# Kernel optimization log

Measured on AMD Instinct MI355X. Metric: run time of the kernel, lower is better.

The kernel has to match this reference:

```python
import jax, jax.numpy as jnp
import numpy as np

EMBED_DIM = 768
NUM_HEADS = 12
LORA_DIM = 64
HEAD_DIM = EMBED_DIM // NUM_HEADS
SCALING = float(HEAD_DIM) ** -0.5


def quick_gelu(x):
    return x * jax.nn.sigmoid(1.702 * x)


def setup_inputs() -> dict:
    key = jax.random.key(0)
    ks = jax.random.split(key, 12)
    bsz, tgt_len, E = 128, 197, EMBED_DIM
    x = jax.random.normal(ks[0], (bsz, tgt_len, E), dtype=jnp.float32)
    attn_mask = jnp.zeros((bsz, tgt_len, tgt_len), dtype=jnp.float32)
    top_idx = jax.random.randint(ks[1], (bsz,), 0, tgt_len)
    s = 0.02
    return {
        "x": x,
        "attn_mask": attn_mask,
        "in_proj_weight": jax.random.normal(ks[2], (3 * E, E)) * s,
        "in_proj_bias": jnp.zeros((3 * E,), jnp.float32),
        "out_proj_weight": jax.random.normal(ks[3], (E, E)) * s,
        "out_proj_bias": jnp.zeros((E,), jnp.float32),
        "lora_a": jax.random.normal(ks[4], (LORA_DIM, E)) * s,
        "lora_b": jax.random.normal(ks[5], (3 * E, LORA_DIM)) * s,
        "down_weight": jax.random.normal(ks[6], (LORA_DIM, E)) * s,
        "down_bias": jax.random.normal(ks[7], (LORA_DIM,)) * 1e-6,
        "up_weight": jax.random.normal(ks[8], (E, LORA_DIM)) * s,
        "up_bias": jnp.zeros((E,), jnp.float32),
        "n_f": 16,
        "top_idx": top_idx,
    }


def reference(x, attn_mask, in_proj_weight, in_proj_bias, out_proj_weight,
              out_proj_bias, lora_a, lora_b, down_weight, down_bias,
              up_weight, up_bias, n_f, top_idx):
    bsz, tgt_len, E = x.shape
    H, hd = NUM_HEADS, HEAD_DIM
    b = bsz // n_f

    # fused QKV + LoRA delta
    qkv = x @ in_proj_weight.T + in_proj_bias          # [bsz, L, 3E]
    qkv = qkv + (x @ lora_a.T) @ lora_b.T              # LoRA delta
    qkv = qkv.reshape(bsz, tgt_len, 3, H, hd)
    qkv = jnp.transpose(qkv, (2, 0, 3, 1, 4))          # [3, bsz, H, L, hd]
    q, k, v = qkv[0], qkv[1], qkv[2]

    # gather per-sample CLS query before scaling (matches torch order)
    q_1 = q[jnp.arange(bsz), :, top_idx, :]            # [bsz, H, hd]
    q_1 = jnp.transpose(q_1.reshape(b, n_f, H, hd), (0, 2, 1, 3))  # [b, H, f, hd]

    # frame-local attention
    attn = jnp.einsum('bhqd,bhkd->bhqk', q * SCALING, k) + attn_mask[:, None, :, :]
    attn = jax.nn.softmax(attn, axis=-1)
    xo = jnp.einsum('bhqk,bhkd->bhqd', attn, v)
    xo = jnp.transpose(xo, (0, 2, 1, 3)).reshape(bsz, tgt_len, E)
    xo = xo @ out_proj_weight.T + out_proj_bias        # [bsz, L, E]

    # global CLS attention over all frames' keys/values
    k_g = jnp.transpose(k.reshape(b, n_f, H, tgt_len, hd), (0, 2, 1, 3, 4)).reshape(b, H, n_f * tgt_len, hd)
    v_g = jnp.transpose(v.reshape(b, n_f, H, tgt_len, hd), (0, 2, 1, 3, 4)).reshape(b, H, n_f * tgt_len, hd)
    mask_g = attn_mask[:, -1, :].reshape(b, n_f * tgt_len)  # [b, f*L]

    attn_1 = jnp.einsum('bhfd,bhkd->bhfk', q_1 * SCALING, k_g) + mask_g[:, None, None, :]
    attn_1 = jax.nn.softmax(attn_1, axis=-1)
    x_1 = jnp.einsum('bhfk,bhkd->bhfd', attn_1, v_g)
    x_1 = jnp.transpose(x_1, (0, 2, 1, 3)).reshape(b, n_f, E)
    x_1 = x_1 @ out_proj_weight.T + out_proj_bias      # [b, f, E]

    # adapter on gathered CLS outputs
    x_0 = xo[jnp.arange(bsz), top_idx, :].reshape(b, n_f, E)
    x_0 = quick_gelu(x_0 @ down_weight.T + down_bias)
    x_0 = x_0 @ up_weight.T + up_bias                  # [b, f, E]

    update_cls = (x_0 + x_1).reshape(bsz, E)
    xo = xo.at[jnp.arange(bsz), top_idx, :].set(update_cls)
    return xo
```

## Files before the change

### kernel.cpp

```cpp
#include <hip/hip_runtime.h>
#include <hip/hip_bf16.h>

typedef __attribute__((ext_vector_type(4))) float f32x4;
typedef __attribute__((ext_vector_type(8))) short s16x8;

#define BSZ 128
#define TGT 197
#define EDIM 768
#define NH 12
#define HD 64
#define NF 16
#define M_TOT (BSZ*TGT)
#define QKV_N (3*EDIM)
#define KG (NF*TGT)
#define VSTR 264
#define NSPL 8
#define KSPL 394
#define LSTR 424

__device__ __forceinline__ float b2f(unsigned short u) {
  return __uint_as_float(((unsigned int)u) << 16);
}
__device__ __forceinline__ float bf2f(__hip_bfloat16 b) { return __bfloat162float(b); }
__device__ __forceinline__ __hip_bfloat16 f2bf(float f) { return __float2bfloat16(f); }
__device__ __forceinline__ unsigned int packbf(float a, float b) {
  __hip_bfloat16 x = __float2bfloat16(a), y = __float2bfloat16(b);
  return (unsigned int)*(unsigned short*)&x | ((unsigned int)*(unsigned short*)&y << 16);
}
__device__ __forceinline__ int swz(int t, int c) {
  return t*64 + (c ^ ((((t & 7) ^ ((t >> 3) & 3))) << 3));
}
__device__ __forceinline__ int vswz(int d, int t) {
  return d*VSTR + (t ^ (d & 56));
}

__device__ __forceinline__ void gload_lds16(const void* gsrc, void* ldst) {
  __builtin_amdgcn_global_load_lds(
      (const __attribute__((address_space(1))) unsigned int*)gsrc,
      (__attribute__((address_space(3))) unsigned int*)ldst, 16, 0, 0);
}

__global__ void detect_dtype(const unsigned short* __restrict__ xraw,
                             int* __restrict__ flag, int* __restrict__ mz) {
  if (threadIdx.x == 0 && blockIdx.x == 0) {
    float mx = 0.f;
    for (int j = 0; j < 1024; ++j) {
      float v = fabsf(b2f(xraw[j]));
      if (v < 1e30f) mx = fmaxf(mx, v);
      else mx = 1e30f;
    }
    *flag = (mx < 100.0f) ? 1 : 0;
    *mz = 1;
  }
}

__global__ __launch_bounds__(256) void detect_mask_zero(
    const unsigned int* __restrict__ mraw, int nelem,
    const int* __restrict__ flag, int* __restrict__ mz)
{
  const int isbf = *flag;
  const int nwords = isbf ? (nelem >> 1) : nelem;
  const unsigned int am = isbf ? 0x7fff7fffu : 0x7fffffffu;
  unsigned int acc = 0;
  for (int i = blockIdx.x*256 + threadIdx.x; i < nwords; i += gridDim.x*256)
    acc |= (mraw[i] & am);
  if (acc) atomicAnd(mz, 0);
}

__global__ __launch_bounds__(256) void convert_bf16(
    const void* __restrict__ src, __hip_bfloat16* __restrict__ dst,
    int n8, const int* __restrict__ flag, int skip_if_bf)
{
  const int isbf = *flag;
  if (skip_if_bf && isbf) return;
  int i = blockIdx.x * 256 + threadIdx.x;
  const int stride = gridDim.x * 256;
  if (isbf) {
    const s16x8* s = (const s16x8*)src;
    s16x8* d = (s16x8*)dst;
    for (; i < n8; i += stride) d[i] = s[i];
  } else {
    const f32x4* s = (const f32x4*)src;
    s16x8* d = (s16x8*)dst;
    for (; i < n8; i += stride) {
      f32x4 a = s[i*2], b = s[i*2+1];
      s16x8 o;
      #pragma unroll
      for (int j = 0; j < 4; ++j) { __hip_bfloat16 t = f2bf(a[j]); o[j] = *(short*)&t; }
      #pragma unroll
      for (int j = 0; j < 4; ++j) { __hip_bfloat16 t = f2bf(b[j]); o[4+j] = *(short*)&t; }
      d[i] = o;
    }
  }
}

struct CvBatch {
  const void* src[10];
  void* dst[10];
  int off8[11];
};

__global__ __launch_bounds__(256) void convert_batch(CvBatch cb, const int* __restrict__ flag)
{
  const int isbf = *flag;
  const int total = cb.off8[10];
  for (int i = blockIdx.x*256 + threadIdx.x; i < total; i += gridDim.x*256) {
    int s = 0;
    #pragma unroll
    for (int k = 1; k < 10; ++k) s += (i >= cb.off8[k]);
    const int li = i - cb.off8[s];
    if (isbf) {
      ((s16x8*)cb.dst[s])[li] = ((const s16x8*)cb.src[s])[li];
    } else {
      const f32x4* sp = (const f32x4*)cb.src[s];
      f32x4 a = sp[li*2], b = sp[li*2+1];
      s16x8 o;
      #pragma unroll
      for (int j = 0; j < 4; ++j) { __hip_bfloat16 t = f2bf(a[j]); o[j] = *(short*)&t; }
      #pragma unroll
      for (int j = 0; j < 4; ++j) { __hip_bfloat16 t = f2bf(b[j]); o[4+j] = *(short*)&t; }
      ((s16x8*)cb.dst[s])[li] = o;
    }
  }
}

__global__ __launch_bounds__(256) void build_wc(
    const __hip_bfloat16* __restrict__ W,
    const __hip_bfloat16* __restrict__ la,
    const __hip_bfloat16* __restrict__ lb,
    __hip_bfloat16* __restrict__ Wc)
{
  __shared__ float lbr[64];
  const int n = blockIdx.x;
  if (threadIdx.x < 64) lbr[threadIdx.x] = bf2f(lb[n*64 + threadIdx.x]);
  __syncthreads();
  for (int e = threadIdx.x; e < EDIM; e += 256) {
    float acc = bf2f(W[(size_t)n*EDIM + e]);
    for (int r = 0; r < 64; ++r) acc += lbr[r] * bf2f(la[r*EDIM + e]);
    Wc[(size_t)n*EDIM + e] = f2bf(acc);
  }
}

__global__ __launch_bounds__(512) void gemm_bt_8ph(
    const __hip_bfloat16* __restrict__ A,
    const __hip_bfloat16* __restrict__ A_alt,
    const __hip_bfloat16* __restrict__ B,
    const __hip_bfloat16* __restrict__ bias,
    void* __restrict__ C,
    int M, int N, int K, int ntiles,
    const int* __restrict__ flag, int flag_mode)
{
  __shared__ char lds[131072];
  const int tid = threadIdx.x;
  const int wave = tid >> 6, lane = tid & 63;
  const int l16 = lane & 15, kq = lane >> 4;
  const int wr = wave >> 2, wc2 = wave & 3;

  const int nwg = gridDim.x;
  const int bid = blockIdx.x;
  const int qc = nwg >> 3, rc = nwg & 7;
  const int xcd = bid & 7;
  const int wgid = (xcd < rc ? xcd*(qc+1) : rc*(qc+1) + (xcd-rc)*qc) + (bid >> 3);
  const long brow = (long)(wgid / ntiles) * 256;
  const long bcol = (long)(wgid % ntiles) * 256;

  const int isbf = *flag;
  const __hip_bfloat16* Ause = isbf ? A_alt : A;
  const int nkt = K >> 6;

  const int srow = tid >> 3;
  const int schunk = tid & 7;
  const int wuni = wave << 10;

  auto stA = [&](int t, int buf, int issue) {
    int ar = issue*64 + srow;
    int cs = schunk ^ (ar & 7);
    long gr = brow + ar; if (gr > (long)M - 1) gr = M - 1;
    gload_lds16(Ause + gr*(long)K + t*64 + cs*8,
                lds + buf*65536 + issue*8192 + wuni);
  };
  auto stB = [&](int t, int buf, int issue) {
    int br = issue*64 + srow;
    int cs = schunk ^ (br & 7);
    gload_lds16(B + (bcol + br)*(long)K + t*64 + cs*8,
                lds + buf*65536 + 32768 + issue*8192 + wuni);
  };
  auto rdA = [&](int buf, int q, int a, int ks) -> s16x8 {
    int ar = wr*128 + q*32 + a*16 + l16;
    int ch = ks*4 + kq;
    return *(const s16x8*)(lds + buf*65536 + ar*128 + ((ch ^ (ar & 7)) << 4));
  };
  auto rdB = [&](int buf, int ni, int ks) -> s16x8 {
    int br = wc2*64 + ni*16 + l16;
    int ch = ks*4 + kq;
    return *(const s16x8*)(lds + buf*65536 + 32768 + br*128 + ((ch ^ (br & 7)) << 4));
  };

  f32x4 acc[8][4];
  #pragma unroll
  for (int i = 0; i < 8; ++i)
    #pragma unroll
    for (int j = 0; j < 4; ++j) acc[i][j] = (f32x4){0.f,0.f,0.f,0.f};

  stB(0,0,0); stB(0,0,1); stB(0,0,2); stB(0,0,3);
  stA(0,0,0); stA(0,0,2); stA(0,0,1); stA(0,0,3);
  asm volatile("s_waitcnt vmcnt(2)" ::: "memory");
  __builtin_amdgcn_s_barrier();

  for (int t = 0; t < nkt; ++t) {
    const int cur = t & 1, nxt = cur ^ 1;
    const bool pf = (t + 1 < nkt);
    s16x8 bfr[4][2], af[2][2];

    #pragma unroll
    for (int ni = 0; ni < 4; ++ni) { bfr[ni][0] = rdB(cur,ni,0); bfr[ni][1] = rdB(cur,ni,1); }
    af[0][0]=rdA(cur,0,0,0); af[0][1]=rdA(cur,0,0,1);
    af[1][0]=rdA(cur,0,1,0); af[1][1]=rdA(cur,0,1,1);
    if (pf) { stB(t+1,nxt,0); stB(t+1,nxt,1); }
    __builtin_amdgcn_s_barrier();
    asm volatile("s_waitcnt lgkmcnt(0)" ::: "memory");
    __builtin_amdgcn_sched_barrier(0);
    __builtin_amdgcn_s_setprio(1);
    #pragma unroll
    for (int ks = 0; ks < 2; ++ks)
      #pragma unroll
      for (int ni = 0; ni < 4; ++ni) {
        acc[0][ni] = __builtin_amdgcn_mfma_f32_16x16x32_bf16(af[0][ks], bfr[ni][ks], acc[0][ni], 0,0,0);
        acc[1][ni] = __builtin_amdgcn_mfma_f32_16x16x32_bf16(af[1][ks], bfr[ni][ks], acc[1][ni], 0,0,0);
      }
    __builtin_amdgcn_s_setprio(0);

    af[0][0]=rdA(cur,1,0,0); af[0][1]=rdA(cur,1,0,1);
    af[1][0]=rdA(cur,1,1,0); af[1][1]=rdA(cur,1,1,1);
    if (pf) {
      stB(t+1,nxt,2); stB(t+1,nxt,3);
      asm volatile("s_waitcnt vmcnt(4)" ::: "memory");
    } else {
      asm volatile("s_waitcnt vmcnt(0)" ::: "memory");
    }
    __builtin_amdgcn_s_barrier();
    asm volatile("s_waitcnt lgkmcnt(0)" ::: "memory");
    __builtin_amdgcn_sched_barrier(0);
    __builtin_amdgcn_s_setprio(1);
    #pragma unroll
    for (int ks = 0; ks < 2; ++ks)
      #pragma unroll
      for (int ni = 0; ni < 4; ++ni) {
        acc[2][ni] = __builtin_amdgcn_mfma_f32_16x16x32_bf16(af[0][ks], bfr[ni][ks], acc[2][ni], 0,0,0);
        acc[3][ni] = __builtin_amdgcn_mfma_f32_16x16x32_bf16(af[1][ks], bfr[ni][ks], acc[3][ni], 0,0,0);
      }
    __builtin_amdgcn_s_setprio(0);

    af[0][0]=rdA(cur,2,0,0); af[0][1]=rdA(cur,2,0,1);
    af[1][0]=rdA(cur,2,1,0); af[1][1]=rdA(cur,2,1,1);
    if (pf) { stA(t+1,nxt,0); stA(t+1,nxt,2); }
    __builtin_amdgcn_s_barrier();
    asm volatile("s_waitcnt lgkmcnt(0)" ::: "memory");
    __builtin_amdgcn_sched_barrier(0);
    __builtin_amdgcn_s_setprio(1);
    #pragma unroll
    for (int ks = 0; ks < 2; ++ks)
      #pragma unroll
      for (int ni = 0; ni < 4; ++ni) {
        acc[4][ni] = __builtin_amdgcn_mfma_f32_16x16x32_bf16(af[0][ks], bfr[ni][ks], acc[4][ni], 0,0,0);
        acc[5][ni] = __builtin_amdgcn_mfma_f32_16x16x32_bf16(af[1][ks], bfr[ni][ks], acc[5][ni], 0,0,0);
      }
    __builtin_amdgcn_s_setprio(0);

    af[0][0]=rdA(cur,3,0,0); af[0][1]=rdA(cur,3,0,1);
    af[1][0]=rdA(cur,3,1,0); af[1][1]=rdA(cur,3,1,1);
    if (pf) { stA(t+1,nxt,1); stA(t+1,nxt,3); }
    asm volatile("s_waitcnt vmcnt(2)" ::: "memory");
    __builtin_amdgcn_s_barrier();
    asm volatile("s_waitcnt lgkmcnt(0)" ::: "memory");
    __builtin_amdgcn_sched_barrier(0);
    __builtin_amdgcn_s_setprio(1);
    #pragma unroll
    for (int ks = 0; ks < 2; ++ks)
      #pragma unroll
      for (int ni = 0; ni < 4; ++ni) {
        acc[6][ni] = __builtin_amdgcn_mfma_f32_16x16x32_bf16(af[0][ks], bfr[ni][ks], acc[6][ni], 0,0,0);
        acc[7][ni] = __builtin_amdgcn_mfma_f32_16x16x32_bf16(af[1][ks], bfr[ni][ks], acc[7][ni], 0,0,0);
      }
    __builtin_amdgcn_s_setprio(0);
  }

  __builtin_amdgcn_s_barrier();

  const int f32o = flag_mode && (!isbf);
  float bv[4];
  #pragma unroll
  for (int ni = 0; ni < 4; ++ni) bv[ni] = bf2f(bias[bcol + wc2*64 + ni*16 + l16]);
  const int o4 = kq*4;

  if (!f32o) {
    __hip_bfloat16* eb = (__hip_bfloat16*)(lds + wave*2048);
    __hip_bfloat16* Cb = (__hip_bfloat16*)C;
    const int rr = lane >> 3, cg = lane & 7;
    #pragma unroll
    for (int mi = 0; mi < 8; ++mi) {
      #pragma unroll
      for (int ni = 0; ni < 4; ++ni)
        #pragma unroll
        for (int r = 0; r < 4; ++r) {
          const int row16 = o4 + r;
          const int sidx = row16*64 + ((((ni*2 + (l16 >> 3)) ^ (row16 & 7)) << 3) | (l16 & 7));
          eb[sidx] = f2bf(acc[mi][ni][r] + bv[ni]);
        }
      asm volatile("s_waitcnt lgkmcnt(0)" ::: "memory");
      __builtin_amdgcn_sched_barrier(0);
      #pragma unroll
      for (int pass = 0; pass < 2; ++pass) {
        const int row16 = pass*8 + rr;
        const long grow = brow + wr*128 + mi*16 + row16;
        if (grow < M) {
          s16x8 v = *(const s16x8*)(eb + row16*64 + ((cg ^ (row16 & 7)) << 3));
          *(s16x8*)(Cb + grow*(long)N + bcol + wc2*64 + cg*8) = v;
        }
      }
      asm volatile("s_waitcnt lgkmcnt(0)" ::: "memory");
      __builtin_amdgcn_sched_barrier(0);
    }
  } else {
    #pragma unroll
    for (int mi = 0; mi < 8; ++mi)
      #pragma unroll
      for (int ni = 0; ni < 4; ++ni)
        #pragma unroll
        for (int r = 0; r < 4; ++r) {
          const long grow = brow + wr*128 + mi*16 + o4 + r;
          if (grow < M)
            ((float*)C)[grow*(long)N + bcol + wc2*64 + ni*16 + l16] = acc[mi][ni][r] + bv[ni];
        }
  }
}

__global__ __launch_bounds__(256) void attn_fused(
    const __hip_bfloat16* __restrict__ qkv,
    const __hip_bfloat16* __restrict__ mask,
    const __hip_bfloat16* __restrict__ mask_raw,
    const int* __restrict__ flag,
    const int* __restrict__ mzp,
    __hip_bfloat16* __restrict__ xop)
{
  __shared__ __hip_bfloat16 lVt[64*VSTR];

  const int tid = threadIdx.x;
  const int blk = blockIdx.x;
  const int xcd = blk & 7;
  const int slot = blk >> 3;
  const int ih = xcd * 192 + (slot >> 2);
  const int qt = slot & 3;
  const int h = ih % NH;
  const int i = ih / NH;
  const int q0 = qt * 64;
  const size_t rowbase = (size_t)i * TGT;
  const int wave = tid >> 6, lane = tid & 63;
  const int l16 = lane & 15, kq = lane >> 4;
  const int mz = *mzp;
  const __hip_bfloat16* msk = (*flag) ? mask_raw : mask;

  int qr = q0 + wave*16 + l16;
  const int qrc = qr > TGT-1 ? TGT-1 : qr;
  s16x8 qf[2];
  #pragma unroll
  for (int kk = 0; kk < 2; ++kk)
    qf[kk] = *(const s16x8*)(qkv + (rowbase + qrc)*QKV_N + h*HD + kk*32 + kq*8);

  const f32x4 z = {0.f,0.f,0.f,0.f};
  for (int idx = tid; idx < 224*8; idx += 256) {
    int t = idx >> 3, c8 = idx & 7;
    f32x4 vv = z;
    if (t < TGT) vv = *(const f32x4*)(qkv + (rowbase + t)*QKV_N + 2*EDIM + h*HD + c8*8);
    const __hip_bfloat16* pv = (const __hip_bfloat16*)&vv;
    const int tx = t ^ (c8 << 3);
    #pragma unroll
    for (int j = 0; j < 8; ++j)
      lVt[(c8*8 + j)*VSTR + tx] = pv[j];
  }
  __syncthreads();

  f32x4 acc[14];
  #pragma unroll
  for (int nf = 0; nf < 14; ++nf) {
    int trow = nf*16 + l16; if (trow > TGT-1) trow = TGT-1;
    acc[nf] = (f32x4){0.f,0.f,0.f,0.f};
    #pragma unroll
    for (int kk = 0; kk < 2; ++kk) {
      s16x8 kf = *(const s16x8*)(qkv + (rowbase + trow)*QKV_N + EDIM + h*HD + kk*32 + kq*8);
      acc[nf] = __builtin_amdgcn_mfma_f32_16x16x32_bf16(kf, qf[kk], acc[nf], 0, 0, 0);
    }
  }

  float mx = -1e30f;
  #pragma unroll
  for (int nf = 0; nf < 14; ++nf) {
    #pragma unroll
    for (int r = 0; r < 4; ++r) {
      const int t = nf*16 + kq*4 + r;
      float s;
      if (t < TGT) {
        s = acc[nf][r]*0.125f;
        if (!mz) s += bf2f(msk[(rowbase + qrc)*TGT + t]);
      } else s = -1e30f;
      acc[nf][r] = s;
      mx = fmaxf(mx, s);
    }
  }
  mx = fmaxf(mx, __shfl_xor(mx, 16));
  mx = fmaxf(mx, __shfl_xor(mx, 32));

  float rs = 0.f;
  unsigned int pk[14][2];
  #pragma unroll
  for (int nf = 0; nf < 14; ++nf) {
    float p0 = __expf(acc[nf][0] - mx);
    float p1 = __expf(acc[nf][1] - mx);
    float p2 = __expf(acc[nf][2] - mx);
    float p3 = __expf(acc[nf][3] - mx);
    rs += (p0 + p1) + (p2 + p3);
    pk[nf][0] = packbf(p0, p1);
    pk[nf][1] = packbf(p2, p3);
  }
  rs += __shfl_xor(rs, 16);
  rs += __shfl_xor(rs, 32);

  f32x4 oacc[4];
  #pragma unroll
  for (int nf = 0; nf < 4; ++nf) oacc[nf] = (f32x4){0.f,0.f,0.f,0.f};

  const int slbase = l16 + ((kq & 1) << 5);
  #pragma unroll
  for (int kt = 0; kt < 7; ++kt) {
    s16x8 pa;
    #pragma unroll
    for (int jp = 0; jp < 4; ++jp) {
      const int srcLane = slbase + ((jp >> 1) << 4);
      int va = __shfl((int)pk[2*kt][jp & 1], srcLane, 64);
      int vb = __shfl((int)pk[2*kt + 1][jp & 1], srcLane, 64);
      int sel = (kq < 2) ? va : vb;
      pa[2*jp]     = (short)(sel & 0xffff);
      pa[2*jp + 1] = (short)(((unsigned int)sel) >> 16);
    }
    #pragma unroll
    for (int nf = 0; nf < 4; ++nf) {
      s16x8 vf = *(const s16x8*)(lVt + vswz(nf*16 + l16, kt*32 + kq*8));
      oacc[nf] = __builtin_amdgcn_mfma_f32_16x16x32_bf16(pa, vf, oacc[nf], 0, 0, 0);
    }
  }

  #pragma unroll
  for (int r = 0; r < 4; ++r) {
    const float rsrc = __shfl(rs, kq*4 + r, 64);
    const int qw = q0 + wave*16 + kq*4 + r;
    if (qw < TGT) {
      const float inv = 1.0f / rsrc;
      #pragma unroll
      for (int nf = 0; nf < 4; ++nf)
        xop[(rowbase + qw)*(size_t)EDIM + h*HD + nf*16 + l16] = f2bf(oacc[nf][r] * inv);
    }
  }
}

__global__ __launch_bounds__(256) void cls_split(
    const __hip_bfloat16* __restrict__ qkv,
    const __hip_bfloat16* __restrict__ mask,
    const __hip_bfloat16* __restrict__ mask_raw,
    const int* __restrict__ flag,
    const int* __restrict__ mzp,
    const int* __restrict__ top_idx,
    float* __restrict__ pO,
    float* __restrict__ pm,
    float* __restrict__ pl)
{
  __shared__ __hip_bfloat16 lQ[16*64];
  __shared__ __hip_bfloat16 lS[16*LSTR];
  __shared__ __hip_bfloat16 lV[256*64];
  __shared__ float red[16][17];
  __shared__ float rmax[16];
  __shared__ float rsum[16];

  const int tid = threadIdx.x;
  const int sp = blockIdx.x & 7;
  const int gh = blockIdx.x >> 3;
  const int g = gh / NH;
  const int h = gh % NH;
  const int k0 = sp * KSPL;
  const int wave = tid >> 6, lane = tid & 63;
  const int l16 = lane & 15, kq = lane >> 4, o4 = (lane >> 4) * 4;
  const int mz = *mzp;
  const __hip_bfloat16* msk = (*flag) ? mask_raw : mask;

  if (tid < 128) {
    int qi = tid >> 3, c8 = tid & 7;
    int ib = g*NF + qi;
    int top = top_idx[ib];
    f32x4 v = *(const f32x4*)(qkv + ((size_t)ib*TGT + top)*QKV_N + h*HD + c8*8);
    *(f32x4*)(lQ + qi*64 + c8*8) = v;
  }
  __syncthreads();

  s16x8 q8[2];
  #pragma unroll
  for (int kk = 0; kk < 2; ++kk)
    q8[kk] = *(const s16x8*)(lQ + l16*64 + kk*32 + kq*8);

  for (int nf = wave; nf < 26; nf += 4) {
    const int keyl = nf*16 + l16;
    const int keyg = k0 + (keyl < KSPL ? keyl : 0);
    f32x4 a = {0.f,0.f,0.f,0.f};
    const size_t krow = (size_t)g*KG + keyg;
    #pragma unroll
    for (int kk = 0; kk < 2; ++kk) {
      s16x8 k8 = *(const s16x8*)(qkv + krow*QKV_N + EDIM + h*HD + kk*32 + kq*8);
      a = __builtin_amdgcn_mfma_f32_16x16x32_bf16(q8[kk], k8, a, 0, 0, 0);
    }
    float mval = 0.f;
    if (!mz && keyl < KSPL) {
      const int f = keyg / 197;
      const int t = keyg - f*197;
      mval = bf2f(msk[((size_t)(g*NF + f)*TGT + (TGT-1))*TGT + t]);
    }
    #pragma unroll
    for (int r = 0; r < 4; ++r)
      lS[(o4 + r)*LSTR + nf*16 + l16] = f2bf(keyl < KSPL ? a[r]*0.125f + mval : -1e30f);
  }
  __syncthreads();

  {
    const int q = tid >> 4, c = tid & 15;
    float mx = -1e30f;
    for (int gch = c; gch < 52; gch += 16) {
      s16x8 sv = *(const s16x8*)(lS + q*LSTR + gch*8);
      #pragma unroll
      for (int j = 0; j < 8; ++j) mx = fmaxf(mx, b2f((unsigned short)sv[j]));
    }
    red[q][c] = mx;
    __syncthreads();
    if (tid < 16) {
      float m = red[tid][0];
      for (int j = 1; j < 16; ++j) m = fmaxf(m, red[tid][j]);
      rmax[tid] = m;
    }
    __syncthreads();
    const float rowmax = rmax[q];
    float sum = 0.f;
    for (int gch = c; gch < 52; gch += 16) {
      s16x8 sv = *(const s16x8*)(lS + q*LSTR + gch*8);
      s16x8 ov;
      #pragma unroll
      for (int jp = 0; jp < 4; ++jp) {
        float e0 = __expf(b2f((unsigned short)sv[2*jp])   - rowmax);
        float e1 = __expf(b2f((unsigned short)sv[2*jp+1]) - rowmax);
        sum += e0 + e1;
        unsigned int pr = packbf(e0, e1);
        ov[2*jp]   = (short)(pr & 0xffff);
        ov[2*jp+1] = (short)(pr >> 16);
      }
      *(s16x8*)(lS + q*LSTR + gch*8) = ov;
    }
    red[q][c] = sum;
    __syncthreads();
    if (tid < 16) {
      float s = 0.f;
      for (int j = 0; j < 16; ++j) s += red[tid][j];
      rsum[tid] = s;
    }
  }

  f32x4 oa = {0.f,0.f,0.f,0.f};
  const f32x4 z = {0.f,0.f,0.f,0.f};
  #pragma unroll
  for (int cki = 0; cki < 2; ++cki) {
    const int ck = cki * 256;
    const int nrows = cki ? 160 : 256;
    const int nks = cki ? 5 : 8;
    __syncthreads();
    for (int idx = tid; idx < nrows*8; idx += 256) {
      int t2 = idx >> 3, c8 = idx & 7;
      int keyl = ck + t2;
      f32x4 v = z;
      if (keyl < KSPL)
        v = *(const f32x4*)(qkv + ((size_t)g*KG + k0 + keyl)*QKV_N + 2*EDIM + h*HD + c8*8);
      *(f32x4*)(lV + swz(t2, c8*8)) = v;
    }
    __syncthreads();
    for (int ks = 0; ks < nks; ++ks) {
      s16x8 pa = *(const s16x8*)(lS + l16*LSTR + ck + ks*32 + kq*8);
      s16x8 vf;
      #pragma unroll
      for (int j = 0; j < 8; ++j) {
        const int t2 = ks*32 + kq*8 + j;
        vf[j] = *(const short*)(lV + swz(t2, wave*16 + l16));
      }
      oa = __builtin_amdgcn_mfma_f32_16x16x32_bf16(pa, vf, oa, 0, 0, 0);
    }
  }

  const int ps = gh*NSPL + sp;
  #pragma unroll
  for (int r = 0; r < 4; ++r)
    pO[((size_t)ps*16 + (o4 + r))*64 + wave*16 + l16] = oa[r];
  if (tid < 16) {
    pm[ps*16 + tid] = rmax[tid];
    pl[ps*16 + tid] = rsum[tid];
  }
}

__global__ __launch_bounds__(256) void cls_combine(
    const float* __restrict__ pO,
    const float* __restrict__ pm,
    const float* __restrict__ pl,
    __hip_bfloat16* __restrict__ x1buf)
{
  __shared__ float M[16];
  __shared__ float L[16];
  __shared__ float sc[NSPL][16];
  const int tid = threadIdx.x;
  const int gh = blockIdx.x;
  const int g = gh / NH;
  const int h = gh % NH;

  if (tid < 16) {
    float m = -1e30f;
    for (int s = 0; s < NSPL; ++s) m = fmaxf(m, pm[(gh*NSPL + s)*16 + tid]);
    M[tid] = m;
  }
  __syncthreads();
  if (tid < 128) {
    const int s = tid >> 4, q = tid & 15;
    sc[s][q] = __expf(pm[(gh*NSPL + s)*16 + q] - M[q]);
  }
  __syncthreads();
  if (tid < 16) {
    float l = 0.f;
    for (int s = 0; s < NSPL; ++s) l += pl[(gh*NSPL + s)*16 + tid] * sc[s][tid];
    L[tid] = l;
  }
  __syncthreads();
  for (int idx = tid; idx < 16*64; idx += 256) {
    const int q = idx >> 6, d = idx & 63;
    float acc = 0.f;
    for (int s = 0; s < NSPL; ++s)
      acc += pO[((size_t)(gh*NSPL + s)*16 + q)*64 + d] * sc[s][q];
    x1buf[((size_t)(g*NF + q))*EDIM + h*64 + d] = f2bf(acc / L[q]);
  }
}

__global__ __launch_bounds__(256) void final_update(
    void* __restrict__ out,
    const __hip_bfloat16* __restrict__ x1p,
    const __hip_bfloat16* __restrict__ dw, const __hip_bfloat16* __restrict__ db,
    const __hip_bfloat16* __restrict__ uw, const __hip_bfloat16* __restrict__ ub,
    const int* __restrict__ top_idx, const int* __restrict__ flag)
{
  __shared__ float x0[EDIM];
  __shared__ float hmid[64];
  const int i = blockIdx.x;
  const int tid = threadIdx.x;
  const int top = top_idx[i];
  const int isbf = *flag;
  const size_t rowoff = ((size_t)i*TGT + top)*EDIM;
  for (int e = tid; e < EDIM; e += 256)
    x0[e] = isbf ? bf2f(((const __hip_bfloat16*)out)[rowoff + e])
                 : ((const float*)out)[rowoff + e];
  __syncthreads();
  if (tid < 64) {
    float a = bf2f(db[tid]);
    for (int e = 0; e < EDIM; ++e) a += x0[e] * bf2f(dw[tid*EDIM + e]);
    hmid[tid] = a / (1.f + __expf(-1.702f * a));
  }
  __syncthreads();
  for (int e = tid; e < EDIM; e += 256) {
    float a = bf2f(ub[e]) + bf2f(x1p[(size_t)i*EDIM + e]);
    #pragma unroll
    for (int r = 0; r < 64; ++r) a += hmid[r] * bf2f(uw[e*64 + r]);
    if (isbf) ((__hip_bfloat16*)out)[rowoff + e] = f2bf(a);
    else ((float*)out)[rowoff + e] = a;
  }
}

extern "C" void kernel_launch(void* const* d_in, const int* in_sizes, int n_in,
                              void* d_out, int out_size, void* d_ws, size_t ws_size,
                              hipStream_t stream) {
  (void)in_sizes; (void)n_in; (void)out_size; (void)ws_size;
  const int* top_idx = (const int*)d_in[13];
  const __hip_bfloat16* x_raw    = (const __hip_bfloat16*)d_in[0];
  const __hip_bfloat16* mask_raw = (const __hip_bfloat16*)d_in[1];

  char* ws = (char*)d_ws;
  size_t off = 0;
  auto alloc = [&](size_t bytes) { char* p = ws + off; off += (bytes + 15) & ~(size_t)15; return p; };

  int* flag = (int*)alloc(16);
  int* mz   = (int*)alloc(16);
  __hip_bfloat16* x_c    = (__hip_bfloat16*)alloc((size_t)19365888*2);
  __hip_bfloat16* mask_c = (__hip_bfloat16*)alloc((size_t)4967552*2);
  __hip_bfloat16* wIn_c  = (__hip_bfloat16*)alloc((size_t)1769472*2);
  __hip_bfloat16* bIn_c  = (__hip_bfloat16*)alloc((size_t)2304*2);
  __hip_bfloat16* wOut_c = (__hip_bfloat16*)alloc((size_t)589824*2);
  __hip_bfloat16* bOut_c = (__hip_bfloat16*)alloc((size_t)768*2);
  __hip_bfloat16* la_c   = (__hip_bfloat16*)alloc((size_t)49152*2);
  __hip_bfloat16* lb_c   = (__hip_bfloat16*)alloc((size_t)147456*2);
  __hip_bfloat16* dw_c   = (__hip_bfloat16*)alloc((size_t)49152*2);
  __hip_bfloat16* db_c   = (__hip_bfloat16*)alloc((size_t)64*2);
  __hip_bfloat16* uw_c   = (__hip_bfloat16*)alloc((size_t)49152*2);
  __hip_bfloat16* ub_c   = (__hip_bfloat16*)alloc((size_t)768*2);
  __hip_bfloat16* Wc     = (__hip_bfloat16*)alloc((size_t)QKV_N*EDIM*2);
  __hip_bfloat16* qkv    = (__hip_bfloat16*)alloc((size_t)M_TOT*QKV_N*2);
  __hip_bfloat16* xop    = (__hip_bfloat16*)alloc((size_t)M_TOT*EDIM*2);
  __hip_bfloat16* x1b    = (__hip_bfloat16*)alloc((size_t)BSZ*EDIM*2);
  __hip_bfloat16* x1p    = (__hip_bfloat16*)alloc((size_t)BSZ*EDIM*2);
  float* pO = (float*)alloc((size_t)96*NSPL*16*64*4);
  float* pm = (float*)alloc((size_t)96*NSPL*16*4);
  float* pl = (float*)alloc((size_t)96*NSPL*16*4);

  detect_dtype<<<1, 64, 0, stream>>>((const unsigned short*)d_in[0], flag, mz);
  detect_mask_zero<<<2048, 256, 0, stream>>>((const unsigned int*)d_in[1], 4967552, flag, mz);

  convert_bf16<<<2048, 256, 0, stream>>>(d_in[0], x_c, 19365888/8, flag, 1);
  convert_bf16<<<2048, 256, 0, stream>>>(d_in[1], mask_c, 4967552/8, flag, 1);

  CvBatch cb;
  const int srcIdx[10] = {2,3,4,5,6,7,8,9,10,11};
  void* dsts[10] = {wIn_c, bIn_c, wOut_c, bOut_c, la_c, lb_c, dw_c, db_c, uw_c, ub_c};
  const int ns[10] = {1769472, 2304, 589824, 768, 49152, 147456, 49152, 64, 49152, 768};
  int cum = 0;
  for (int k = 0; k < 10; ++k) {
    cb.src[k] = d_in[srcIdx[k]];
    cb.dst[k] = dsts[k];
    cb.off8[k] = cum;
    cum += ns[k] / 8;
  }
  cb.off8[10] = cum;
  convert_batch<<<(cum + 255)/256, 256, 0, stream>>>(cb, flag);

  build_wc<<<2304, 256, 0, stream>>>(wIn_c, la_c, lb_c, Wc);

  gemm_bt_8ph<<<99*9, 512, 0, stream>>>(x_c, x_raw, Wc, bIn_c, qkv,
                                        M_TOT, QKV_N, EDIM, 9, flag, 0);
  attn_fused<<<dim3(6144), 256, 0, stream>>>(qkv, mask_c, mask_raw, flag, mz, xop);
  cls_split<<<dim3(96*NSPL), 256, 0, stream>>>(qkv, mask_c, mask_raw, flag, mz,
                                               top_idx, pO, pm, pl);
  gemm_bt_8ph<<<99*3, 512, 0, stream>>>(xop, xop, wOut_c, bOut_c, d_out,
                                        M_TOT, EDIM, EDIM, 3, flag, 1);
  cls_combine<<<dim3(96), 256, 0, stream>>>(pO, pm, pl, x1b);
  gemm_bt_8ph<<<3, 512, 0, stream>>>(x1b, x1b, wOut_c, bOut_c, x1p,
                                     BSZ, EDIM, EDIM, 3, flag, 0);
  final_update<<<128, 256, 0, stream>>>(d_out, x1p, dw_c, db_c, uw_c, ub_c, top_idx, flag);
}
```

Measured before the change: 469.9 us.

## Merge out-projection GEMM and CLS split attention into one heterogeneous launch

Combines the out-projection GEMM and the split-K CLS global attention into one kernel. The first 297 blocks run the GEMM and the rest run the CLS split work, so the small CLS workload fills CUs left idle by the GEMM tail and one launch is removed. In exchange, the CLS blocks now use 512-thread blocks with half the threads idle and inherit the GEMM's 128KB shared-memory allocation, which may lower occupancy for that part.

After: 462.7 us. About the same (-1.5%).

```diff
diff --git a/kernel.cpp b/kernel.cpp
--- a/kernel.cpp
+++ b/kernel.cpp
@@ -17,6 +17,7 @@
 #define NSPL 8
 #define KSPL 394
 #define LSTR 424
+#define NGEMM_OP 297
 
 __device__ __forceinline__ float b2f(unsigned short u) {
   return __uint_as_float(((unsigned int)u) << 16);
@@ -335,6 +336,348 @@
   }
 }
 
+__global__ __launch_bounds__(512) void outproj_cls(
+    const __hip_bfloat16* __restrict__ A,
+    const __hip_bfloat16* __restrict__ B,
+    const __hip_bfloat16* __restrict__ bias,
+    void* __restrict__ C,
+    const __hip_bfloat16* __restrict__ qkv,
+    const __hip_bfloat16* __restrict__ mask,
+    const __hip_bfloat16* __restrict__ mask_raw,
+    const int* __restrict__ flag,
+    const int* __restrict__ mzp,
+    const int* __restrict__ top_idx,
+    float* __restrict__ pO,
+    float* __restrict__ pm,
+    float* __restrict__ pl)
+{
+  __shared__ char lds[131072];
+  const int tid = threadIdx.x;
+  const int wave = tid >> 6, lane = tid & 63;
+  const int l16 = lane & 15, kq = lane >> 4;
+  const int isbf = *flag;
+
+  if (blockIdx.x < NGEMM_OP) {
+    const int wr = wave >> 2, wc2 = wave & 3;
+    const int M = M_TOT, N = EDIM, K = EDIM, ntiles = 3;
+    const int nwg = NGEMM_OP;
+    const int bid = blockIdx.x;
+    const int qc = nwg >> 3, rc = nwg & 7;
+    const int xcd = bid & 7;
+    const int wgid = (xcd < rc ? xcd*(qc+1) : rc*(qc+1) + (xcd-rc)*qc) + (bid >> 3);
+    const long brow = (long)(wgid / ntiles) * 256;
+    const long bcol = (long)(wgid % ntiles) * 256;
+    const int nkt = K >> 6;
+
+    const int srow = tid >> 3;
+    const int schunk = tid & 7;
+    const int wuni = wave << 10;
+
+    auto stA = [&](int t, int buf, int issue) {
+      int ar = issue*64 + srow;
+      int cs = schunk ^ (ar & 7);
+      long gr = brow + ar; if (gr > (long)M - 1) gr = M - 1;
+      gload_lds16(A + gr*(long)K + t*64 + cs*8,
+                  lds + buf*65536 + issue*8192 + wuni);
+    };
+    auto stB = [&](int t, int buf, int issue) {
+      int br = issue*64 + srow;
+      int cs = schunk ^ (br & 7);
+      gload_lds16(B + (bcol + br)*(long)K + t*64 + cs*8,
+                  lds + buf*65536 + 32768 + issue*8192 + wuni);
+    };
+    auto rdA = [&](int buf, int q, int a, int ks) -> s16x8 {
+      int ar = wr*128 + q*32 + a*16 + l16;
+      int ch = ks*4 + kq;
+      return *(const s16x8*)(lds + buf*65536 + ar*128 + ((ch ^ (ar & 7)) << 4));
+    };
+    auto rdB = [&](int buf, int ni, int ks) -> s16x8 {
+      int br = wc2*64 + ni*16 + l16;
+      int ch = ks*4 + kq;
+      return *(const s16x8*)(lds + buf*65536 + 32768 + br*128 + ((ch ^ (br & 7)) << 4));
+    };
+
+    f32x4 acc[8][4];
+    #pragma unroll
+    for (int i = 0; i < 8; ++i)
+      #pragma unroll
+      for (int j = 0; j < 4; ++j) acc[i][j] = (f32x4){0.f,0.f,0.f,0.f};
+
+    stB(0,0,0); stB(0,0,1); stB(0,0,2); stB(0,0,3);
+    stA(0,0,0); stA(0,0,2); stA(0,0,1); stA(0,0,3);
+    asm volatile("s_waitcnt vmcnt(2)" ::: "memory");
+    __builtin_amdgcn_s_barrier();
+
+    for (int t = 0; t < nkt; ++t) {
+      const int cur = t & 1, nxt = cur ^ 1;
+      const bool pf = (t + 1 < nkt);
+      s16x8 bfr[4][2], af[2][2];
+
+      #pragma unroll
+      for (int ni = 0; ni < 4; ++ni) { bfr[ni][0] = rdB(cur,ni,0); bfr[ni][1] = rdB(cur,ni,1); }
+      af[0][0]=rdA(cur,0,0,0); af[0][1]=rdA(cur,0,0,1);
+      af[1][0]=rdA(cur,0,1,0); af[1][1]=rdA(cur,0,1,1);
+      if (pf) { stB(t+1,nxt,0); stB(t+1,nxt,1); }
+      __builtin_amdgcn_s_barrier();
+      asm volatile("s_waitcnt lgkmcnt(0)" ::: "memory");
+      __builtin_amdgcn_sched_barrier(0);
+      __builtin_amdgcn_s_setprio(1);
+      #pragma unroll
+      for (int ks = 0; ks < 2; ++ks)
+        #pragma unroll
+        for (int ni = 0; ni < 4; ++ni) {
+          acc[0][ni] = __builtin_amdgcn_mfma_f32_16x16x32_bf16(af[0][ks], bfr[ni][ks], acc[0][ni], 0,0,0);
+          acc[1][ni] = __builtin_amdgcn_mfma_f32_16x16x32_bf16(af[1][ks], bfr[ni][ks], acc[1][ni], 0,0,0);
+        }
+      __builtin_amdgcn_s_setprio(0);
+
+      af[0][0]=rdA(cur,1,0,0); af[0][1]=rdA(cur,1,0,1);
+      af[1][0]=rdA(cur,1,1,0); af[1][1]=rdA(cur,1,1,1);
+      if (pf) {
+        stB(t+1,nxt,2); stB(t+1,nxt,3);
+        asm volatile("s_waitcnt vmcnt(4)" ::: "memory");
+      } else {
+        asm volatile("s_waitcnt vmcnt(0)" ::: "memory");
+      }
+      __builtin_amdgcn_s_barrier();
+      asm volatile("s_waitcnt lgkmcnt(0)" ::: "memory");
+      __builtin_amdgcn_sched_barrier(0);
+      __builtin_amdgcn_s_setprio(1);
+      #pragma unroll
+      for (int ks = 0; ks < 2; ++ks)
+        #pragma unroll
+        for (int ni = 0; ni < 4; ++ni) {
+          acc[2][ni] = __builtin_amdgcn_mfma_f32_16x16x32_bf16(af[0][ks], bfr[ni][ks], acc[2][ni], 0,0,0);
+          acc[3][ni] = __builtin_amdgcn_mfma_f32_16x16x32_bf16(af[1][ks], bfr[ni][ks], acc[3][ni], 0,0,0);
+        }
+      __builtin_amdgcn_s_setprio(0);
+
+      af[0][0]=rdA(cur,2,0,0); af[0][1]=rdA(cur,2,0,1);
+      af[1][0]=rdA(cur,2,1,0); af[1][1]=rdA(cur,2,1,1);
+      if (pf) { stA(t+1,nxt,0); stA(t+1,nxt,2); }
+      __builtin_amdgcn_s_barrier();
+      asm volatile("s_waitcnt lgkmcnt(0)" ::: "memory");
+      __builtin_amdgcn_sched_barrier(0);
+      __builtin_amdgcn_s_setprio(1);
+      #pragma unroll
+      for (int ks = 0; ks < 2; ++ks)
+        #pragma unroll
+        for (int ni = 0; ni < 4; ++ni) {
+          acc[4][ni] = __builtin_amdgcn_mfma_f32_16x16x32_bf16(af[0][ks], bfr[ni][ks], acc[4][ni], 0,0,0);
+          acc[5][ni] = __builtin_amdgcn_mfma_f32_16x16x32_bf16(af[1][ks], bfr[ni][ks], acc[5][ni], 0,0,0);
+        }
+      __builtin_amdgcn_s_setprio(0);
+
+      af[0][0]=rdA(cur,3,0,0); af[0][1]=rdA(cur,3,0,1);
+      af[1][0]=rdA(cur,3,1,0); af[1][1]=rdA(cur,3,1,1);
+      if (pf) { stA(t+1,nxt,1); stA(t+1,nxt,3); }
+      asm volatile("s_waitcnt vmcnt(2)" ::: "memory");
+      __builtin_amdgcn_s_barrier();
+      asm volatile("s_waitcnt lgkmcnt(0)" ::: "memory");
+      __builtin_amdgcn_sched_barrier(0);
+      __builtin_amdgcn_s_setprio(1);
+      #pragma unroll
+      for (int ks = 0; ks < 2; ++ks)
+        #pragma unroll
+        for (int ni = 0; ni < 4; ++ni) {
+          acc[6][ni] = __builtin_amdgcn_mfma_f32_16x16x32_bf16(af[0][ks], bfr[ni][ks], acc[6][ni], 0,0,0);
+          acc[7][ni] = __builtin_amdgcn_mfma_f32_16x16x32_bf16(af[1][ks], bfr[ni][ks], acc[7][ni], 0,0,0);
+        }
+      __builtin_amdgcn_s_setprio(0);
+    }
+
+    __builtin_amdgcn_s_barrier();
+
+    float bv[4];
+    #pragma unroll
+    for (int ni = 0; ni < 4; ++ni) bv[ni] = bf2f(bias[bcol + wc2*64 + ni*16 + l16]);
+    const int o4 = kq*4;
+
+    if (isbf) {
+      __hip_bfloat16* eb = (__hip_bfloat16*)(lds + wave*2048);
+      __hip_bfloat16* Cb = (__hip_bfloat16*)C;
+      const int rr = lane >> 3, cg = lane & 7;
+      #pragma unroll
+      for (int mi = 0; mi < 8; ++mi) {
+        #pragma unroll
+        for (int ni = 0; ni < 4; ++ni)
+          #pragma unroll
+          for (int r = 0; r < 4; ++r) {
+            const int row16 = o4 + r;
+            const int sidx = row16*64 + ((((ni*2 + (l16 >> 3)) ^ (row16 & 7)) << 3) | (l16 & 7));
+            eb[sidx] = f2bf(acc[mi][ni][r] + bv[ni]);
+          }
+        asm volatile("s_waitcnt lgkmcnt(0)" ::: "memory");
+        __builtin_amdgcn_sched_barrier(0);
+        #pragma unroll
+        for (int pass = 0; pass < 2; ++pass) {
+          const int row16 = pass*8 + rr;
+          const long grow = brow + wr*128 + mi*16 + row16;
+          if (grow < M) {
+            s16x8 v = *(const s16x8*)(eb + row16*64 + ((cg ^ (row16 & 7)) << 3));
+            *(s16x8*)(Cb + grow*(long)N + bcol + wc2*64 + cg*8) = v;
+          }
+        }
+        asm volatile("s_waitcnt lgkmcnt(0)" ::: "memory");
+        __builtin_amdgcn_sched_barrier(0);
+      }
+    } else {
+      #pragma unroll
+      for (int mi = 0; mi < 8; ++mi)
+        #pragma unroll
+        for (int ni = 0; ni < 4; ++ni)
+          #pragma unroll
+          for (int r = 0; r < 4; ++r) {
+            const long grow = brow + wr*128 + mi*16 + o4 + r;
+            if (grow < M)
+              ((float*)C)[grow*(long)N + bcol + wc2*64 + ni*16 + l16] = acc[mi][ni][r] + bv[ni];
+          }
+    }
+  } else {
+    __hip_bfloat16* lQ = (__hip_bfloat16*)lds;
+    __hip_bfloat16* lS = lQ + 16*64;
+    __hip_bfloat16* lV = lS + 16*LSTR;
+    float* red  = (float*)(lds + 49152);
+    float* rmax = (float*)(lds + 50304);
+    float* rsum = (float*)(lds + 50368);
+
+    const int cb = blockIdx.x - NGEMM_OP;
+    const int sp = cb & 7;
+    const int gh = cb >> 3;
+    const int g = gh / NH;
+    const int h = gh % NH;
+    const int k0 = sp * KSPL;
+    const int o4 = kq * 4;
+    const int mz = *mzp;
+    const __hip_bfloat16* msk = isbf ? mask_raw : mask;
+
+    if (tid < 128) {
+      int qi = tid >> 3, c8 = tid & 7;
+      int ib = g*NF + qi;
+      int top = top_idx[ib];
+      f32x4 v = *(const f32x4*)(qkv + ((size_t)ib*TGT + top)*QKV_N + h*HD + c8*8);
+      *(f32x4*)(lQ + qi*64 + c8*8) = v;
+    }
+    __syncthreads();
+
+    if (wave < 4) {
+      s16x8 q8[2];
+      #pragma unroll
+      for (int kk = 0; kk < 2; ++kk)
+        q8[kk] = *(const s16x8*)(lQ + l16*64 + kk*32 + kq*8);
+
+      for (int nf = wave; nf < 26; nf += 4) {
+        const int keyl = nf*16 + l16;
+        const int keyg = k0 + (keyl < KSPL ? keyl : 0);
+        f32x4 a = {0.f,0.f,0.f,0.f};
+        const size_t krow = (size_t)g*KG + keyg;
+        #pragma unroll
+        for (int kk = 0; kk < 2; ++kk) {
+          s16x8 k8 = *(const s16x8*)(qkv + krow*QKV_N + EDIM + h*HD + kk*32 + kq*8);
+          a = __builtin_amdgcn_mfma_f32_16x16x32_bf16(q8[kk], k8, a, 0, 0, 0);
+        }
+        float mval = 0.f;
+        if (!mz && keyl < KSPL) {
+          const int f = keyg / 197;
+          const int t = keyg - f*197;
+          mval = bf2f(msk[((size_t)(g*NF + f)*TGT + (TGT-1))*TGT + t]);
+        }
+        #pragma unroll
+        for (int r = 0; r < 4; ++r)
+          lS[(o4 + r)*LSTR + nf*16 + l16] = f2bf(keyl < KSPL ? a[r]*0.125f + mval : -1e30f);
+      }
+    }
+    __syncthreads();
+
+    {
+      const int q = tid >> 4, c = tid & 15;
+      if (tid < 256) {
+        float mx = -1e30f;
+        for (int gch = c; gch < 52; gch += 16) {
+          s16x8 sv = *(const s16x8*)(lS + q*LSTR + gch*8);
+          #pragma unroll
+          for (int j = 0; j < 8; ++j) mx = fmaxf(mx, b2f((unsigned short)sv[j]));
+        }
+        red[q*17 + c] = mx;
+      }
+      __syncthreads();
+      if (tid < 16) {
+        float m = red[tid*17];
+        for (int j = 1; j < 16; ++j) m = fmaxf(m, red[tid*17 + j]);
+        rmax[tid] = m;
+      }
+      __syncthreads();
+      if (tid < 256) {
+        const float rowmax = rmax[q];
+        float sum = 0.f;
+        for (int gch = c; gch < 52; gch += 16) {
+          s16x8 sv = *(const s16x8*)(lS + q*LSTR + gch*8);
+          s16x8 ov;
+          #pragma unroll
+          for (int jp = 0; jp < 4; ++jp) {
+            float e0 = __expf(b2f((unsigned short)sv[2*jp])   - rowmax);
+            float e1 = __expf(b2f((unsigned short)sv[2*jp+1]) - rowmax);
+            sum += e0 + e1;
+            unsigned int pr = packbf(e0, e1);
+            ov[2*jp]   = (short)(pr & 0xffff);
+            ov[2*jp+1] = (short)(pr >> 16);
+          }
+          *(s16x8*)(lS + q*LSTR + gch*8) = ov;
+        }
+        red[q*17 + c] = sum;
+      }
+      __syncthreads();
+      if (tid < 16) {
+        float s = 0.f;
+        for (int j = 0; j < 16; ++j) s += red[tid*17 + j];
+        rsum[tid] = s;
+      }
+    }
+
+    f32x4 oa = {0.f,0.f,0.f,0.f};
+    const f32x4 z = {0.f,0.f,0.f,0.f};
+    #pragma unroll
+    for (int cki = 0; cki < 2; ++cki) {
+      const int ck = cki * 256;
+      const int nrows = cki ? 160 : 256;
+      const int nks = cki ? 5 : 8;
+      __syncthreads();
+      for (int idx = tid; idx < nrows*8; idx += 512) {
+        int t2 = idx >> 3, c8 = idx & 7;
+        int keyl = ck + t2;
+        f32x4 v = z;
+        if (keyl < KSPL)
+          v = *(const f32x4*)(qkv + ((size_t)g*KG + k0 + keyl)*QKV_N + 2*EDIM + h*HD + c8*8);
+        *(f32x4*)(lV + swz(t2, c8*8)) = v;
+      }
+      __syncthreads();
+      if (tid < 256) {
+        for (int ks = 0; ks < nks; ++ks) {
+          s16x8 pa = *(const s16x8*)(lS + l16*LSTR + ck + ks*32 + kq*8);
+          s16x8 vf;
+          #pragma unroll
+          for (int j = 0; j < 8; ++j) {
+            const int t2 = ks*32 + kq*8 + j;
+            vf[j] = *(const short*)(lV + swz(t2, wave*16 + l16));
+          }
+          oa = __builtin_amdgcn_mfma_f32_16x16x32_bf16(pa, vf, oa, 0, 0, 0);
+        }
+      }
+    }
+
+    if (tid < 256) {
+      const int ps = gh*NSPL + sp;
+      #pragma unroll
+      for (int r = 0; r < 4; ++r)
+        pO[((size_t)ps*16 + (o4 + r))*64 + wave*16 + l16] = oa[r];
+      if (tid < 16) {
+        pm[ps*16 + tid] = rmax[tid];
+        pl[ps*16 + tid] = rsum[tid];
+      }
+    }
+  }
+}
+
 __global__ __launch_bounds__(256) void attn_fused(
     const __hip_bfloat16* __restrict__ qkv,
     const __hip_bfloat16* __restrict__ mask,
@@ -459,151 +802,6 @@
       for (int nf = 0; nf < 4; ++nf)
         xop[(rowbase + qw)*(size_t)EDIM + h*HD + nf*16 + l16] = f2bf(oacc[nf][r] * inv);
     }
-  }
-}
-
-__global__ __launch_bounds__(256) void cls_split(
-    const __hip_bfloat16* __restrict__ qkv,
-    const __hip_bfloat16* __restrict__ mask,
-    const __hip_bfloat16* __restrict__ mask_raw,
-    const int* __restrict__ flag,
-    const int* __restrict__ mzp,
-    const int* __restrict__ top_idx,
-    float* __restrict__ pO,
-    float* __restrict__ pm,
-    float* __restrict__ pl)
-{
-  __shared__ __hip_bfloat16 lQ[16*64];
-  __shared__ __hip_bfloat16 lS[16*LSTR];
-  __shared__ __hip_bfloat16 lV[256*64];
-  __shared__ float red[16][17];
-  __shared__ float rmax[16];
-  __shared__ float rsum[16];
-
-  const int tid = threadIdx.x;
-  const int sp = blockIdx.x & 7;
-  const int gh = blockIdx.x >> 3;
-  const int g = gh / NH;
-  const int h = gh % NH;
-  const int k0 = sp * KSPL;
-  const int wave = tid >> 6, lane = tid & 63;
-  const int l16 = lane & 15, kq = lane >> 4, o4 = (lane >> 4) * 4;
-  const int mz = *mzp;
-  const __hip_bfloat16* msk = (*flag) ? mask_raw : mask;
-
-  if (tid < 128) {
-    int qi = tid >> 3, c8 = tid & 7;
-    int ib = g*NF + qi;
-    int top = top_idx[ib];
-    f32x4 v = *(const f32x4*)(qkv + ((size_t)ib*TGT + top)*QKV_N + h*HD + c8*8);
-    *(f32x4*)(lQ + qi*64 + c8*8) = v;
-  }
-  __syncthreads();
-
-  s16x8 q8[2];
-  #pragma unroll
-  for (int kk = 0; kk < 2; ++kk)
-    q8[kk] = *(const s16x8*)(lQ + l16*64 + kk*32 + kq*8);
-
-  for (int nf = wave; nf < 26; nf += 4) {
-    const int keyl = nf*16 + l16;
-    const int keyg = k0 + (keyl < KSPL ? keyl : 0);
-    f32x4 a = {0.f,0.f,0.f,0.f};
-    const size_t krow = (size_t)g*KG + keyg;
-    #pragma unroll
-    for (int kk = 0; kk < 2; ++kk) {
-      s16x8 k8 = *(const s16x8*)(qkv + krow*QKV_N + EDIM + h*HD + kk*32 + kq*8);
-      a = __builtin_amdgcn_mfma_f32_16x16x32_bf16(q8[kk], k8, a, 0, 0, 0);
-    }
-    float mval = 0.f;
-    if (!mz && keyl < KSPL) {
-      const int f = keyg / 197;
-      const int t = keyg - f*197;
-      mval = bf2f(msk[((size_t)(g*NF + f)*TGT + (TGT-1))*TGT + t]);
-    }
-    #pragma unroll
-    for (int r = 0; r < 4; ++r)
-      lS[(o4 + r)*LSTR + nf*16 + l16] = f2bf(keyl < KSPL ? a[r]*0.125f + mval : -1e30f);
-  }
-  __syncthreads();
-
-  {
-    const int q = tid >> 4, c = tid & 15;
-    float mx = -1e30f;
-    for (int gch = c; gch < 52; gch += 16) {
-      s16x8 sv = *(const s16x8*)(lS + q*LSTR + gch*8);
-      #pragma unroll
-      for (int j = 0; j < 8; ++j) mx = fmaxf(mx, b2f((unsigned short)sv[j]));
-    }
-    red[q][c] = mx;
-    __syncthreads();
-    if (tid < 16) {
-      float m = red[tid][0];
-      for (int j = 1; j < 16; ++j) m = fmaxf(m, red[tid][j]);
-      rmax[tid] = m;
-    }
-    __syncthreads();
-    const float rowmax = rmax[q];
-    float sum = 0.f;
-    for (int gch = c; gch < 52; gch += 16) {
-      s16x8 sv = *(const s16x8*)(lS + q*LSTR + gch*8);
-      s16x8 ov;
-      #pragma unroll
-      for (int jp = 0; jp < 4; ++jp) {
-        float e0 = __expf(b2f((unsigned short)sv[2*jp])   - rowmax);
-        float e1 = __expf(b2f((unsigned short)sv[2*jp+1]) - rowmax);
-        sum += e0 + e1;
-        unsigned int pr = packbf(e0, e1);
-        ov[2*jp]   = (short)(pr & 0xffff);
-        ov[2*jp+1] = (short)(pr >> 16);
-      }
-      *(s16x8*)(lS + q*LSTR + gch*8) = ov;
-    }
-    red[q][c] = sum;
-    __syncthreads();
-    if (tid < 16) {
-      float s = 0.f;
-      for (int j = 0; j < 16; ++j) s += red[tid][j];
-      rsum[tid] = s;
-    }
-  }
-
-  f32x4 oa = {0.f,0.f,0.f,0.f};
-  const f32x4 z = {0.f,0.f,0.f,0.f};
-  #pragma unroll
-  for (int cki = 0; cki < 2; ++cki) {
-    const int ck = cki * 256;
-    const int nrows = cki ? 160 : 256;
-    const int nks = cki ? 5 : 8;
-    __syncthreads();
-    for (int idx = tid; idx < nrows*8; idx += 256) {
-      int t2 = idx >> 3, c8 = idx & 7;
-      int keyl = ck + t2;
-      f32x4 v = z;
-      if (keyl < KSPL)
-        v = *(const f32x4*)(qkv + ((size_t)g*KG + k0 + keyl)*QKV_N + 2*EDIM + h*HD + c8*8);
-      *(f32x4*)(lV + swz(t2, c8*8)) = v;
-    }
-    __syncthreads();
-    for (int ks = 0; ks < nks; ++ks) {
-      s16x8 pa = *(const s16x8*)(lS + l16*LSTR + ck + ks*32 + kq*8);
-      s16x8 vf;
-      #pragma unroll
-      for (int j = 0; j < 8; ++j) {
-        const int t2 = ks*32 + kq*8 + j;
-        vf[j] = *(const short*)(lV + swz(t2, wave*16 + l16));
-      }
-      oa = __builtin_amdgcn_mfma_f32_16x16x32_bf16(pa, vf, oa, 0, 0, 0);
-    }
-  }
-
-  const int ps = gh*NSPL + sp;
-  #pragma unroll
-  for (int r = 0; r < 4; ++r)
-    pO[((size_t)ps*16 + (o4 + r))*64 + wave*16 + l16] = oa[r];
-  if (tid < 16) {
-    pm[ps*16 + tid] = rmax[tid];
-    pl[ps*16 + tid] = rsum[tid];
   }
 }
 
@@ -740,10 +938,9 @@
   gemm_bt_8ph<<<99*9, 512, 0, stream>>>(x_c, x_raw, Wc, bIn_c, qkv,
                                         M_TOT, QKV_N, EDIM, 9, flag, 0);
   attn_fused<<<dim3(6144), 256, 0, stream>>>(qkv, mask_c, mask_raw, flag, mz, xop);
-  cls_split<<<dim3(96*NSPL), 256, 0, stream>>>(qkv, mask_c, mask_raw, flag, mz,
-                                               top_idx, pO, pm, pl);
-  gemm_bt_8ph<<<99*3, 512, 0, stream>>>(xop, xop, wOut_c, bOut_c, d_out,
-                                        M_TOT, EDIM, EDIM, 3, flag, 1);
+  outproj_cls<<<dim3(NGEMM_OP + 96*NSPL), 512, 0, stream>>>(
+      xop, wOut_c, bOut_c, d_out,
+      qkv, mask_c, mask_raw, flag, mz, top_idx, pO, pm, pl);
   cls_combine<<<dim3(96), 256, 0, stream>>>(pO, pm, pl, x1b);
   gemm_bt_8ph<<<3, 512, 0, stream>>>(x1b, x1b, wOut_c, bOut_c, x1p,
                                      BSZ, EDIM, EDIM, 3, flag, 0);
```
